# Performance work log

Hardware: AMD Instinct MI355X
Metric: run time of the kernel (lower is better)

The kernel has to match this reference:

```python
import jax, jax.numpy as jnp
import numpy as np

D_MODEL = 1024
N_HEADS = 16
D_K = D_MODEL // N_HEADS
NEG = -1e10


def setup_inputs() -> dict:
    key = jax.random.key(0)
    ks = jax.random.split(key, 12)
    bs, sl = 2, 2048
    q = jax.random.normal(ks[0], (bs, sl, D_MODEL), dtype=jnp.float32)
    k = jax.random.normal(ks[1], (bs, sl, D_MODEL), dtype=jnp.float32)
    v = jax.random.normal(ks[2], (bs, sl, D_MODEL), dtype=jnp.float32)
    mask = jax.random.randint(ks[3], (bs, 1, sl, sl), 0, 2).astype(bool)
    s = 1.0 / np.sqrt(D_MODEL)
    Wq = jax.random.uniform(ks[4], (D_MODEL, D_MODEL), jnp.float32, -s, s)
    bq = jax.random.uniform(ks[5], (D_MODEL,), jnp.float32, -s, s)
    Wk = jax.random.uniform(ks[6], (D_MODEL, D_MODEL), jnp.float32, -s, s)
    bk = jax.random.uniform(ks[7], (D_MODEL,), jnp.float32, -s, s)
    Wv = jax.random.uniform(ks[8], (D_MODEL, D_MODEL), jnp.float32, -s, s)
    bv = jax.random.uniform(ks[9], (D_MODEL,), jnp.float32, -s, s)
    Wo = jax.random.uniform(ks[10], (D_MODEL, D_MODEL), jnp.float32, -s, s)
    bo = jax.random.uniform(ks[11], (D_MODEL,), jnp.float32, -s, s)
    return {"q": q, "k": k, "v": v, "mask": mask,
            "Wq": Wq, "bq": bq, "Wk": Wk, "bk": bk,
            "Wv": Wv, "bv": bv, "Wo": Wo, "bo": bo}


def reference(q, k, v, mask, Wq, bq, Wk, bk, Wv, bv, Wo, bo):
    bs, sl, _ = q.shape
    sl2 = k.shape[1]
    # linear projections (torch Linear: x @ W.T + b), split into heads: [b, h, s, d_k]
    qh = (q @ Wq.T + bq).reshape(bs, sl, N_HEADS, D_K).transpose(0, 2, 1, 3)
    kh = (k @ Wk.T + bk).reshape(bs, sl2, N_HEADS, D_K).transpose(0, 2, 1, 3)
    vh = (v @ Wv.T + bv).reshape(bs, sl2, N_HEADS, D_K).transpose(0, 2, 1, 3)
    scores = jnp.einsum('bhqd,bhkd->bhqk', qh, kh) / jnp.sqrt(jnp.float32(D_K))
    scores = jnp.where(mask, NEG, scores)
    attn = jax.nn.softmax(scores, axis=-1)
    z = jnp.einsum('bhqk,bhkd->bhqd', attn, vh)  # [b, h, sl, d_k]
    z = z.transpose(0, 2, 1, 3).reshape(bs, sl, D_MODEL)
    return z @ Wo.T + bo
```

## Files before the change

### kernel.cpp

```cpp
#include <hip/hip_runtime.h>

typedef __attribute__((ext_vector_type(8))) short short8;
typedef __attribute__((ext_vector_type(4))) float f32x4;

#define MFMA16(a, b, c) __builtin_amdgcn_mfma_f32_16x16x32_bf16((a), (b), (c), 0, 0, 0)

#if __has_builtin(__builtin_amdgcn_exp2f)
#define EXP2(x) __builtin_amdgcn_exp2f(x)
#else
#define EXP2(x) __expf((x) * 0.6931471805599453f)
#endif

__device__ __forceinline__ unsigned short f2bf(float f) {
  unsigned int u = __float_as_uint(f);
  u += 0x7FFFu + ((u >> 16) & 1u);
  return (unsigned short)(u >> 16);
}

__device__ __forceinline__ void gload16(const void* g, void* l) {
  __builtin_amdgcn_global_load_lds((const __attribute__((address_space(1))) void*)g,
                                   (__attribute__((address_space(3))) void*)l, 16, 0, 0);
}

__device__ __forceinline__ short8 fragld64(const unsigned short* base, int row, int kchunk) {
  int cc = kchunk ^ (row & 7);
  return *(const short8*)(base + row * 64 + cc * 8);
}

__device__ __forceinline__ short8 vfragld(const unsigned short* base, int row, int kchunk) {
  int cc = kchunk ^ (row & 7) ^ ((row >> 3) & 7);
  return *(const short8*)(base + row * 64 + cc * 8);
}

__global__ void cvt3(const float* __restrict__ a, const float* __restrict__ b,
                     const float* __restrict__ c, unsigned short* __restrict__ out, int n4) {
  const float* src = (blockIdx.z == 0) ? a : ((blockIdx.z == 1) ? b : c);
  int i = blockIdx.x * blockDim.x + threadIdx.x;
  if (i >= n4) return;
  float4 v = ((const float4*)src)[i];
  ushort4 o;
  o.x = f2bf(v.x); o.y = f2bf(v.y); o.z = f2bf(v.z); o.w = f2bf(v.w);
  ((ushort4*)(out + (size_t)blockIdx.z * (size_t)n4 * 4))[i] = o;
}

__global__ void cvt4(const float* __restrict__ a, const float* __restrict__ b,
                     const float* __restrict__ c, const float* __restrict__ d,
                     unsigned short* __restrict__ out, int n4) {
  const float* src = (blockIdx.z == 0) ? a : ((blockIdx.z == 1) ? b
                   : ((blockIdx.z == 2) ? c : d));
  int i = blockIdx.x * blockDim.x + threadIdx.x;
  if (i >= n4) return;
  float4 v = ((const float4*)src)[i];
  ushort4 o;
  o.x = f2bf(v.x); o.y = f2bf(v.y); o.z = f2bf(v.z); o.w = f2bf(v.w);
  ((ushort4*)(out + (size_t)blockIdx.z * (size_t)n4 * 4))[i] = o;
}

__global__ void maskpack(const int* __restrict__ m, unsigned long long* __restrict__ mw) {
  const int lane = threadIdx.x & 63;
  const size_t wbase = ((size_t)blockIdx.x * (blockDim.x >> 6) + (threadIdx.x >> 6)) * 4ull;
#pragma unroll
  for (int u = 0; u < 4; ++u) {
    size_t word = wbase + u;
    int x = m[word * 64 + lane];
    unsigned long long bb = __ballot(x != 0);
    if (lane == 0) mw[word] = bb;
  }
}

template<bool OUT_BF16>
__global__ __launch_bounds__(256, 3) void gemm_bt(
    const unsigned short* __restrict__ Abase, const unsigned short* __restrict__ Bbase,
    const float* __restrict__ bias0, const float* __restrict__ bias1,
    const float* __restrict__ bias2, void* __restrict__ outv, float scale0)
{
  constexpr int K = 1024, N = 1024;
  const int z = blockIdx.z;
  const unsigned short* A = Abase + (size_t)z * 4194304ull;
  const unsigned short* B = Bbase + (size_t)z * 1048576ull;
  const float* bias = (z == 0) ? bias0 : ((z == 1) ? bias1 : bias2);
  const float scale = (z == 0) ? scale0 : 1.0f;

  __shared__ unsigned short ldsA[128 * 64];
  __shared__ unsigned short ldsB[128 * 64];

  const int tid = threadIdx.x;
  const int lane = tid & 63, wid = tid >> 6;
  const int c16 = lane & 15, g = lane >> 4;
  const int m0 = blockIdx.y * 128, n0 = blockIdx.x * 128;
  const int wr = (wid >> 1) * 64, wc = (wid & 1) * 64;

  f32x4 acc[4][4] = {};

  for (int kt = 0; kt < K; kt += 64) {
    __syncthreads();
#pragma unroll
    for (int i = 0; i < 4; ++i) {
      int row = i * 32 + (tid >> 3);
      int cc = tid & 7;
      int scc = cc ^ (row & 7);
      gload16(A + (size_t)(m0 + row) * K + kt + scc * 8, ldsA + row * 64 + cc * 8);
      gload16(B + (size_t)(n0 + row) * K + kt + scc * 8, ldsB + row * 64 + cc * 8);
    }
    __syncthreads();
#pragma unroll
    for (int kc = 0; kc < 2; ++kc) {
      short8 af[4], bf[4];
#pragma unroll
      for (int mi = 0; mi < 4; ++mi) af[mi] = fragld64(ldsA, wr + mi * 16 + c16, kc * 4 + g);
#pragma unroll
      for (int ni = 0; ni < 4; ++ni) bf[ni] = fragld64(ldsB, wc + ni * 16 + c16, kc * 4 + g);
#pragma unroll
      for (int mi = 0; mi < 4; ++mi)
#pragma unroll
        for (int ni = 0; ni < 4; ++ni)
          acc[mi][ni] = MFMA16(af[mi], bf[ni], acc[mi][ni]);
    }
  }

#pragma unroll
  for (int mi = 0; mi < 4; ++mi)
#pragma unroll
    for (int ni = 0; ni < 4; ++ni) {
      int col = n0 + wc + ni * 16 + c16;
      float bb = bias[col];
#pragma unroll
      for (int r = 0; r < 4; ++r) {
        int row = m0 + wr + mi * 16 + g * 4 + r;
        float v = (acc[mi][ni][r] + bb) * scale;
        if constexpr (OUT_BF16)
          ((unsigned short*)outv)[(size_t)z * 4194304ull + (size_t)row * N + col] = f2bf(v);
        else
          ((float*)outv)[(size_t)row * N + col] = v;
      }
    }
}

__global__ __launch_bounds__(512, 4) void attn(
    const unsigned short* __restrict__ qh, const unsigned short* __restrict__ kh,
    const unsigned short* __restrict__ vh, const unsigned long long* __restrict__ mw,
    unsigned short* __restrict__ zout)
{
  constexpr int SL = 2048, DM = 1024, NT = SL / 64;
  const int q0 = blockIdx.x * 128;
  const int h = blockIdx.y, b = blockIdx.z;
  const int tid = threadIdx.x, lane = tid & 63, w = tid >> 6;
  const int c16 = lane & 15, g = lane >> 4;

  __shared__ unsigned short kbuf[2][4096];
  __shared__ unsigned short vt[2][4096];
  __shared__ unsigned short pbuf[8][1024];

  const int qa = q0 + w * 16;
  const size_t qoff = ((size_t)b * SL + qa + c16) * DM + (size_t)h * 64;
  short8 qf0 = *(const short8*)(qh + qoff + g * 8);
  short8 qf1 = *(const short8*)(qh + qoff + 32 + g * 8);

  f32x4 zacc[4] = {};
  float mrun = -INFINITY, lrun = 0.f;

  const size_t kvbase = (size_t)b * SL * DM + (size_t)h * 64;
  const unsigned long long* mwq = mw + ((size_t)b * SL + qa + c16) * (SL / 64);

  const int krow = tid >> 3, kcc = tid & 7;
  const int vj = tid >> 3, vd0 = (tid & 7) * 8;

  unsigned long long mwc = mwq[0];
  short8 vr;

  gload16(kh + kvbase + (size_t)krow * DM + (kcc ^ (krow & 7)) * 8,
          kbuf[0] + krow * 64 + kcc * 8);
  vr = *(const short8*)(vh + kvbase + (size_t)vj * DM + vd0);
#pragma unroll
  for (int e = 0; e < 8; ++e) {
    int row = vd0 + e;
    int slot = (vj >> 3) ^ (row & 7) ^ ((row >> 3) & 7);
    vt[0][row * 64 + slot * 8 + (vj & 7)] = (unsigned short)vr[e];
  }

  for (int t = 0; t < NT; ++t) {
    const int cur = t & 1, nxt = cur ^ 1;
    __syncthreads();

    const bool more = (t + 1 < NT);
    unsigned long long mwn = 0;
    if (more) {
      const size_t kb = kvbase + (size_t)(t + 1) * 64 * DM;
      gload16(kh + kb + (size_t)krow * DM + (kcc ^ (krow & 7)) * 8,
              kbuf[nxt] + krow * 64 + kcc * 8);
      vr = *(const short8*)(vh + kb + (size_t)vj * DM + vd0);
      mwn = mwq[t + 1];
    }

    f32x4 sacc[4];
#pragma unroll
    for (int nt = 0; nt < 4; ++nt) {
      unsigned int nib = (unsigned int)(mwc >> (nt * 16 + g * 4)) & 0xFu;
#pragma unroll
      for (int r = 0; r < 4; ++r)
        sacc[nt][r] = ((nib >> r) & 1u) ? -1e10f : 0.0f;
    }
#pragma unroll
    for (int kc = 0; kc < 2; ++kc) {
      short8 qfc = kc ? qf1 : qf0;
#pragma unroll
      for (int nt = 0; nt < 4; ++nt) {
        short8 kf = fragld64(kbuf[cur], nt * 16 + c16, kc * 4 + g);
        sacc[nt] = MFMA16(kf, qfc, sacc[nt]);
      }
    }

    float mx;
    {
      float a0 = fmaxf(fmaxf(sacc[0][0], sacc[0][1]), fmaxf(sacc[0][2], sacc[0][3]));
      float a1 = fmaxf(fmaxf(sacc[1][0], sacc[1][1]), fmaxf(sacc[1][2], sacc[1][3]));
      float a2 = fmaxf(fmaxf(sacc[2][0], sacc[2][1]), fmaxf(sacc[2][2], sacc[2][3]));
      float a3 = fmaxf(fmaxf(sacc[3][0], sacc[3][1]), fmaxf(sacc[3][2], sacc[3][3]));
      mx = fmaxf(fmaxf(a0, a1), fmaxf(a2, a3));
    }
    mx = fmaxf(mx, __shfl_xor(mx, 16));
    mx = fmaxf(mx, __shfl_xor(mx, 32));

    const bool defer = __all(mx <= mrun + 8.f) != 0;
    float mnew = defer ? mrun : fmaxf(mrun, mx);
    float rs;
    {
      float ps[4];
#pragma unroll
      for (int nt = 0; nt < 4; ++nt) {
        float p0 = EXP2(sacc[nt][0] - mnew);
        float p1 = EXP2(sacc[nt][1] - mnew);
        float p2 = EXP2(sacc[nt][2] - mnew);
        float p3 = EXP2(sacc[nt][3] - mnew);
        sacc[nt][0] = p0; sacc[nt][1] = p1; sacc[nt][2] = p2; sacc[nt][3] = p3;
        ps[nt] = (p0 + p1) + (p2 + p3);
      }
      rs = (ps[0] + ps[1]) + (ps[2] + ps[3]);
    }
    rs += __shfl_xor(rs, 16);
    rs += __shfl_xor(rs, 32);
    if (defer) {
      lrun += rs;
    } else {
      float alpha = EXP2(mrun - mnew);
      mrun = mnew;
      lrun = lrun * alpha + rs;
#pragma unroll
      for (int r = 0; r < 4; ++r) {
        float ar = __shfl(alpha, g * 4 + r);
        zacc[0][r] *= ar; zacc[1][r] *= ar; zacc[2][r] *= ar; zacc[3][r] *= ar;
      }
    }

    {
      unsigned short* pbw = pbuf[w];
#pragma unroll
      for (int nt = 0; nt < 4; ++nt) {
        int key0 = nt * 16 + g * 4;
        int a16 = c16 * 64 + (((key0 >> 3) ^ (c16 & 7)) * 8) + (key0 & 7);
        unsigned long long pk =
            (unsigned long long)f2bf(sacc[nt][0])
          | ((unsigned long long)f2bf(sacc[nt][1]) << 16)
          | ((unsigned long long)f2bf(sacc[nt][2]) << 32)
          | ((unsigned long long)f2bf(sacc[nt][3]) << 48);
        *(unsigned long long*)(pbw + a16) = pk;
      }
    }

#pragma unroll
    for (int kc = 0; kc < 2; ++kc) {
      short8 pf = fragld64(pbuf[w], c16, kc * 4 + g);
#pragma unroll
      for (int dt = 0; dt < 4; ++dt) {
        short8 vf = vfragld(vt[cur], dt * 16 + c16, kc * 4 + g);
        zacc[dt] = MFMA16(pf, vf, zacc[dt]);
      }
    }

    if (more) {
#pragma unroll
      for (int e = 0; e < 8; ++e) {
        int row = vd0 + e;
        int slot = (vj >> 3) ^ (row & 7) ^ ((row >> 3) & 7);
        vt[nxt][row * 64 + slot * 8 + (vj & 7)] = (unsigned short)vr[e];
      }
      mwc = mwn;
    }
  }

  float invl = 1.f / lrun;
#pragma unroll
  for (int r = 0; r < 4; ++r) {
    float ir = __shfl(invl, g * 4 + r);
    size_t orow = ((size_t)b * SL + qa + g * 4 + r) * DM + (size_t)h * 64;
#pragma unroll
    for (int dt = 0; dt < 4; ++dt)
      zout[orow + dt * 16 + c16] = f2bf(zacc[dt][r] * ir);
  }
}

extern "C" void kernel_launch(void* const* d_in, const int* in_sizes, int n_in,
                              void* d_out, int out_size, void* d_ws, size_t ws_size,
                              hipStream_t stream) {
  const float* q  = (const float*)d_in[0];
  const float* k  = (const float*)d_in[1];
  const float* v  = (const float*)d_in[2];
  const int* mask = (const int*)d_in[3];
  const float* Wq = (const float*)d_in[4];
  const float* bq = (const float*)d_in[5];
  const float* Wk = (const float*)d_in[6];
  const float* bk = (const float*)d_in[7];
  const float* Wv = (const float*)d_in[8];
  const float* bv = (const float*)d_in[9];
  const float* Wo = (const float*)d_in[10];
  const float* bo = (const float*)d_in[11];

  char* ws = (char*)d_ws;
  unsigned short* xbf = (unsigned short*)ws;
  unsigned long long* mwb = (unsigned long long*)ws;
  unsigned short* wbf = (unsigned short*)(ws + 25165824);
  unsigned short* qkv = (unsigned short*)(ws + 33554432);
  unsigned short* zbf = (unsigned short*)(ws + 58720256);

  cvt3<<<dim3(4096, 1, 3), 256, 0, stream>>>(q, k, v, xbf, 1048576);
  cvt4<<<dim3(1024, 1, 4), 256, 0, stream>>>(Wq, Wk, Wv, Wo, wbf, 262144);

  gemm_bt<true><<<dim3(8, 32, 3), 256, 0, stream>>>(xbf, wbf, bq, bk, bv, (void*)qkv,
                                                    0.125f * 1.44269504088896f);
  maskpack<<<8192, 256, 0, stream>>>(mask, mwb);
  attn<<<dim3(16, 16, 2), 512, 0, stream>>>(qkv, qkv + 4194304ull, qkv + 8388608ull, mwb, zbf);
  gemm_bt<false><<<dim3(8, 32, 1), 256, 0, stream>>>(zbf, wbf + 3145728ull, bo, bo, bo, d_out, 1.0f);
}
```

Baseline: 169.6 us.

## Rework attention kernel around 32x32x16 MFMA with 32 queries per wave

The attention kernel switches from 16x16x32 to 32x32x16 bf16 MFMA. Each wave now owns 32 query rows, and blocks shrink from 512 to 128 threads while the grid doubles. The V transpose layout is simplified, P is packed with v_cvt_pk_bf16_f32, and s_setprio is raised around the MFMA sections. This is meant to cut LDS fragment loads and shuffle overhead per FLOP, at the cost of more registers per wave, fewer waves per block, and more K/V staging work per thread.

```diff
diff --git a/kernel.cpp b/kernel.cpp
--- a/kernel.cpp
+++ b/kernel.cpp
@@ -2,8 +2,10 @@
 
 typedef __attribute__((ext_vector_type(8))) short short8;
 typedef __attribute__((ext_vector_type(4))) float f32x4;
+typedef __attribute__((ext_vector_type(16))) float f32x16;
 
 #define MFMA16(a, b, c) __builtin_amdgcn_mfma_f32_16x16x32_bf16((a), (b), (c), 0, 0, 0)
+#define MFMA32(a, b, c) __builtin_amdgcn_mfma_f32_32x32x16_bf16((a), (b), (c), 0, 0, 0)
 
 #if __has_builtin(__builtin_amdgcn_exp2f)
 #define EXP2(x) __builtin_amdgcn_exp2f(x)
@@ -17,6 +19,16 @@
   return (unsigned short)(u >> 16);
 }
 
+__device__ __forceinline__ unsigned int cvtpk(float lo, float hi) {
+  unsigned int r;
+  asm("v_cvt_pk_bf16_f32 %0, %1, %2" : "=v"(r) : "v"(lo), "v"(hi));
+  return r;
+}
+
+__device__ __forceinline__ float fmax3(float a, float b, float c) {
+  return fmaxf(fmaxf(a, b), c);
+}
+
 __device__ __forceinline__ void gload16(const void* g, void* l) {
   __builtin_amdgcn_global_load_lds((const __attribute__((address_space(1))) void*)g,
                                    (__attribute__((address_space(3))) void*)l, 16, 0, 0);
@@ -24,11 +36,6 @@
 
 __device__ __forceinline__ short8 fragld64(const unsigned short* base, int row, int kchunk) {
   int cc = kchunk ^ (row & 7);
-  return *(const short8*)(base + row * 64 + cc * 8);
-}
-
-__device__ __forceinline__ short8 vfragld(const unsigned short* base, int row, int kchunk) {
-  int cc = kchunk ^ (row & 7) ^ ((row >> 3) & 7);
   return *(const short8*)(base + row * 64 + cc * 8);
 }
 
@@ -136,47 +143,58 @@
     }
 }
 
-__global__ __launch_bounds__(512, 4) void attn(
+__global__ __launch_bounds__(128, 2) void attn(
     const unsigned short* __restrict__ qh, const unsigned short* __restrict__ kh,
     const unsigned short* __restrict__ vh, const unsigned long long* __restrict__ mw,
     unsigned short* __restrict__ zout)
 {
   constexpr int SL = 2048, DM = 1024, NT = SL / 64;
-  const int q0 = blockIdx.x * 128;
   const int h = blockIdx.y, b = blockIdx.z;
   const int tid = threadIdx.x, lane = tid & 63, w = tid >> 6;
-  const int c16 = lane & 15, g = lane >> 4;
+  const int ql = lane & 31;
+  const int hd = lane >> 5;
+  const int qa = blockIdx.x * 64 + w * 32;
 
   __shared__ unsigned short kbuf[2][4096];
   __shared__ unsigned short vt[2][4096];
-  __shared__ unsigned short pbuf[8][1024];
-
-  const int qa = q0 + w * 16;
-  const size_t qoff = ((size_t)b * SL + qa + c16) * DM + (size_t)h * 64;
-  short8 qf0 = *(const short8*)(qh + qoff + g * 8);
-  short8 qf1 = *(const short8*)(qh + qoff + 32 + g * 8);
-
-  f32x4 zacc[4] = {};
+  __shared__ unsigned short pbuf[2][2048];
+
+  short8 qf[4];
+  {
+    const size_t qrow = ((size_t)b * SL + qa + ql) * DM + (size_t)h * 64 + hd * 8;
+#pragma unroll
+    for (int kc = 0; kc < 4; ++kc)
+      qf[kc] = *(const short8*)(qh + qrow + kc * 16);
+  }
+
+  f32x16 zacc0 = {}, zacc1 = {};
   float mrun = -INFINITY, lrun = 0.f;
 
   const size_t kvbase = (size_t)b * SL * DM + (size_t)h * 64;
-  const unsigned long long* mwq = mw + ((size_t)b * SL + qa + c16) * (SL / 64);
-
-  const int krow = tid >> 3, kcc = tid & 7;
-  const int vj = tid >> 3, vd0 = (tid & 7) * 8;
+  const unsigned long long* mwq = mw + ((size_t)b * SL + qa + ql) * (SL / 64);
+
+  const int kr0 = tid >> 3, kcc = tid & 7;
+  const int vkey = tid & 63, vdc0 = tid >> 6;
 
   unsigned long long mwc = mwq[0];
-  short8 vr;
-
-  gload16(kh + kvbase + (size_t)krow * DM + (kcc ^ (krow & 7)) * 8,
-          kbuf[0] + krow * 64 + kcc * 8);
-  vr = *(const short8*)(vh + kvbase + (size_t)vj * DM + vd0);
-#pragma unroll
-  for (int e = 0; e < 8; ++e) {
-    int row = vd0 + e;
-    int slot = (vj >> 3) ^ (row & 7) ^ ((row >> 3) & 7);
-    vt[0][row * 64 + slot * 8 + (vj & 7)] = (unsigned short)vr[e];
-  }
+  short8 vr[4];
+
+#pragma unroll
+  for (int i = 0; i < 4; ++i) {
+    int row = kr0 + 16 * i;
+    gload16(kh + kvbase + (size_t)row * DM + (kcc ^ (row & 7)) * 8,
+            kbuf[0] + row * 64 + kcc * 8);
+  }
+#pragma unroll
+  for (int i = 0; i < 4; ++i)
+    vr[i] = *(const short8*)(vh + kvbase + (size_t)vkey * DM + (vdc0 + 2 * i) * 8);
+#pragma unroll
+  for (int i = 0; i < 4; ++i)
+#pragma unroll
+    for (int e = 0; e < 8; ++e) {
+      int row = (vdc0 + 2 * i) * 8 + e;
+      vt[0][row * 64 + (((vkey >> 3) ^ (row & 7)) * 8) + (vkey & 7)] = (unsigned short)vr[i][e];
+    }
 
   for (int t = 0; t < NT; ++t) {
     const int cur = t & 1, nxt = cur ^ 1;
@@ -186,59 +204,85 @@
     unsigned long long mwn = 0;
     if (more) {
       const size_t kb = kvbase + (size_t)(t + 1) * 64 * DM;
-      gload16(kh + kb + (size_t)krow * DM + (kcc ^ (krow & 7)) * 8,
-              kbuf[nxt] + krow * 64 + kcc * 8);
-      vr = *(const short8*)(vh + kb + (size_t)vj * DM + vd0);
+#pragma unroll
+      for (int i = 0; i < 4; ++i) {
+        int row = kr0 + 16 * i;
+        gload16(kh + kb + (size_t)row * DM + (kcc ^ (row & 7)) * 8,
+                kbuf[nxt] + row * 64 + kcc * 8);
+      }
+#pragma unroll
+      for (int i = 0; i < 4; ++i)
+        vr[i] = *(const short8*)(vh + kb + (size_t)vkey * DM + (vdc0 + 2 * i) * 8);
       mwn = mwq[t + 1];
     }
 
-    f32x4 sacc[4];
-#pragma unroll
-    for (int nt = 0; nt < 4; ++nt) {
-      unsigned int nib = (unsigned int)(mwc >> (nt * 16 + g * 4)) & 0xFu;
-#pragma unroll
-      for (int r = 0; r < 4; ++r)
-        sacc[nt][r] = ((nib >> r) & 1u) ? -1e10f : 0.0f;
-    }
-#pragma unroll
-    for (int kc = 0; kc < 2; ++kc) {
-      short8 qfc = kc ? qf1 : qf0;
-#pragma unroll
-      for (int nt = 0; nt < 4; ++nt) {
-        short8 kf = fragld64(kbuf[cur], nt * 16 + c16, kc * 4 + g);
-        sacc[nt] = MFMA16(kf, qfc, sacc[nt]);
+    unsigned int b0 = ((unsigned int)mwc) >> (hd * 4);
+    unsigned int b1 = ((unsigned int)(mwc >> 32)) >> (hd * 4);
+    f32x16 s0, s1;
+#pragma unroll
+    for (int m = 0; m < 4; ++m) {
+      unsigned int n0 = (b0 >> (m * 8)) & 0xFu;
+      unsigned int n1 = (b1 >> (m * 8)) & 0xFu;
+#pragma unroll
+      for (int c = 0; c < 4; ++c) {
+        s0[m * 4 + c] = ((n0 >> c) & 1u) ? -1e10f : 0.0f;
+        s1[m * 4 + c] = ((n1 >> c) & 1u) ? -1e10f : 0.0f;
       }
     }
+
+    __builtin_amdgcn_s_setprio(1);
+#pragma unroll
+    for (int kc = 0; kc < 4; ++kc) {
+      short8 kf0 = fragld64(kbuf[cur], ql, kc * 2 + hd);
+      short8 kf1 = fragld64(kbuf[cur], 32 + ql, kc * 2 + hd);
+      s0 = MFMA32(kf0, qf[kc], s0);
+      s1 = MFMA32(kf1, qf[kc], s1);
+    }
+    __builtin_amdgcn_s_setprio(0);
 
     float mx;
     {
-      float a0 = fmaxf(fmaxf(sacc[0][0], sacc[0][1]), fmaxf(sacc[0][2], sacc[0][3]));
-      float a1 = fmaxf(fmaxf(sacc[1][0], sacc[1][1]), fmaxf(sacc[1][2], sacc[1][3]));
-      float a2 = fmaxf(fmaxf(sacc[2][0], sacc[2][1]), fmaxf(sacc[2][2], sacc[2][3]));
-      float a3 = fmaxf(fmaxf(sacc[3][0], sacc[3][1]), fmaxf(sacc[3][2], sacc[3][3]));
-      mx = fmaxf(fmaxf(a0, a1), fmaxf(a2, a3));
-    }
-    mx = fmaxf(mx, __shfl_xor(mx, 16));
+      float t0 = fmax3(s0[0], s0[1], s0[2]);
+      float t1 = fmax3(s0[3], s0[4], s0[5]);
+      float t2 = fmax3(s0[6], s0[7], s0[8]);
+      float t3 = fmax3(s0[9], s0[10], s0[11]);
+      float t4 = fmax3(s0[12], s0[13], s0[14]);
+      float t5 = fmax3(s0[15], s1[0], s1[1]);
+      float t6 = fmax3(s1[2], s1[3], s1[4]);
+      float t7 = fmax3(s1[5], s1[6], s1[7]);
+      float t8 = fmax3(s1[8], s1[9], s1[10]);
+      float t9 = fmax3(s1[11], s1[12], s1[13]);
+      float ta = fmaxf(s1[14], s1[15]);
+      float u0 = fmax3(t0, t1, t2);
+      float u1 = fmax3(t3, t4, t5);
+      float u2 = fmax3(t6, t7, t8);
+      float u3 = fmaxf(t9, ta);
+      mx = fmaxf(fmax3(u0, u1, u2), u3);
+    }
     mx = fmaxf(mx, __shfl_xor(mx, 32));
 
-    const bool defer = __all(mx <= mrun + 8.f) != 0;
-    float mnew = defer ? mrun : fmaxf(mrun, mx);
+    const bool defer = (__all(mx <= mrun + 8.f) != 0);
+    const float mnew = defer ? mrun : fmaxf(mrun, mx);
+
+#pragma unroll
+    for (int i = 0; i < 16; ++i) {
+      s0[i] = EXP2(s0[i] - mnew);
+      s1[i] = EXP2(s1[i] - mnew);
+    }
     float rs;
     {
-      float ps[4];
-#pragma unroll
-      for (int nt = 0; nt < 4; ++nt) {
-        float p0 = EXP2(sacc[nt][0] - mnew);
-        float p1 = EXP2(sacc[nt][1] - mnew);
-        float p2 = EXP2(sacc[nt][2] - mnew);
-        float p3 = EXP2(sacc[nt][3] - mnew);
-        sacc[nt][0] = p0; sacc[nt][1] = p1; sacc[nt][2] = p2; sacc[nt][3] = p3;
-        ps[nt] = (p0 + p1) + (p2 + p3);
-      }
-      rs = (ps[0] + ps[1]) + (ps[2] + ps[3]);
-    }
-    rs += __shfl_xor(rs, 16);
+      float a0 = (s0[0] + s0[1]) + (s0[2] + s0[3]);
+      float a1 = (s0[4] + s0[5]) + (s0[6] + s0[7]);
+      float a2 = (s0[8] + s0[9]) + (s0[10] + s0[11]);
+      float a3 = (s0[12] + s0[13]) + (s0[14] + s0[15]);
+      float a4 = (s1[0] + s1[1]) + (s1[2] + s1[3]);
+      float a5 = (s1[4] + s1[5]) + (s1[6] + s1[7]);
+      float a6 = (s1[8] + s1[9]) + (s1[10] + s1[11]);
+      float a7 = (s1[12] + s1[13]) + (s1[14] + s1[15]);
+      rs = ((a0 + a1) + (a2 + a3)) + ((a4 + a5) + (a6 + a7));
+    }
     rs += __shfl_xor(rs, 32);
+
     if (defer) {
       lrun += rs;
     } else {
@@ -246,56 +290,64 @@
       mrun = mnew;
       lrun = lrun * alpha + rs;
 #pragma unroll
-      for (int r = 0; r < 4; ++r) {
-        float ar = __shfl(alpha, g * 4 + r);
-        zacc[0][r] *= ar; zacc[1][r] *= ar; zacc[2][r] *= ar; zacc[3][r] *= ar;
+      for (int reg = 0; reg < 16; ++reg) {
+        float ar = __shfl(alpha, (reg & 3) + 8 * (reg >> 2) + 4 * hd);
+        zacc0[reg] *= ar;
+        zacc1[reg] *= ar;
       }
     }
 
     {
       unsigned short* pbw = pbuf[w];
 #pragma unroll
-      for (int nt = 0; nt < 4; ++nt) {
-        int key0 = nt * 16 + g * 4;
-        int a16 = c16 * 64 + (((key0 >> 3) ^ (c16 & 7)) * 8) + (key0 & 7);
-        unsigned long long pk =
-            (unsigned long long)f2bf(sacc[nt][0])
-          | ((unsigned long long)f2bf(sacc[nt][1]) << 16)
-          | ((unsigned long long)f2bf(sacc[nt][2]) << 32)
-          | ((unsigned long long)f2bf(sacc[nt][3]) << 48);
-        *(unsigned long long*)(pbw + a16) = pk;
-      }
-    }
-
-#pragma unroll
-    for (int kc = 0; kc < 2; ++kc) {
-      short8 pf = fragld64(pbuf[w], c16, kc * 4 + g);
-#pragma unroll
-      for (int dt = 0; dt < 4; ++dt) {
-        short8 vf = vfragld(vt[cur], dt * 16 + c16, kc * 4 + g);
-        zacc[dt] = MFMA16(pf, vf, zacc[dt]);
-      }
-    }
+      for (int st = 0; st < 2; ++st)
+#pragma unroll
+        for (int m = 0; m < 4; ++m) {
+          uint2 pk;
+          if (st == 0) {
+            pk.x = cvtpk(s0[m * 4 + 0], s0[m * 4 + 1]);
+            pk.y = cvtpk(s0[m * 4 + 2], s0[m * 4 + 3]);
+          } else {
+            pk.x = cvtpk(s1[m * 4 + 0], s1[m * 4 + 1]);
+            pk.y = cvtpk(s1[m * 4 + 2], s1[m * 4 + 3]);
+          }
+          int chunk = st * 4 + m;
+          int a16 = ql * 64 + ((chunk ^ (ql & 7)) * 8) + hd * 4;
+          *(uint2*)(pbw + a16) = pk;
+        }
+    }
+
+    __builtin_amdgcn_s_setprio(1);
+#pragma unroll
+    for (int kc = 0; kc < 4; ++kc) {
+      short8 pf = fragld64(pbuf[w], ql, kc * 2 + hd);
+      short8 vf0 = fragld64(vt[cur], ql, kc * 2 + hd);
+      short8 vf1 = fragld64(vt[cur], 32 + ql, kc * 2 + hd);
+      zacc0 = MFMA32(pf, vf0, zacc0);
+      zacc1 = MFMA32(pf, vf1, zacc1);
+    }
+    __builtin_amdgcn_s_setprio(0);
 
     if (more) {
 #pragma unroll
-      for (int e = 0; e < 8; ++e) {
-        int row = vd0 + e;
-        int slot = (vj >> 3) ^ (row & 7) ^ ((row >> 3) & 7);
-        vt[nxt][row * 64 + slot * 8 + (vj & 7)] = (unsigned short)vr[e];
-      }
+      for (int i = 0; i < 4; ++i)
+#pragma unroll
+        for (int e = 0; e < 8; ++e) {
+          int row = (vdc0 + 2 * i) * 8 + e;
+          vt[nxt][row * 64 + (((vkey >> 3) ^ (row & 7)) * 8) + (vkey & 7)] = (unsigned short)vr[i][e];
+        }
       mwc = mwn;
     }
   }
 
   float invl = 1.f / lrun;
 #pragma unroll
-  for (int r = 0; r < 4; ++r) {
-    float ir = __shfl(invl, g * 4 + r);
-    size_t orow = ((size_t)b * SL + qa + g * 4 + r) * DM + (size_t)h * 64;
-#pragma unroll
-    for (int dt = 0; dt < 4; ++dt)
-      zout[orow + dt * 16 + c16] = f2bf(zacc[dt][r] * ir);
+  for (int reg = 0; reg < 16; ++reg) {
+    int qrow = (reg & 3) + 8 * (reg >> 2) + 4 * hd;
+    float il = __shfl(invl, qrow);
+    size_t orow = ((size_t)b * SL + qa + qrow) * DM + (size_t)h * 64;
+    zout[orow + ql] = f2bf(zacc0[reg] * il);
+    zout[orow + 32 + ql] = f2bf(zacc1[reg] * il);
   }
 }
 
@@ -328,6 +380,6 @@
   gemm_bt<true><<<dim3(8, 32, 3), 256, 0, stream>>>(xbf, wbf, bq, bk, bv, (void*)qkv,
                                                     0.125f * 1.44269504088896f);
   maskpack<<<8192, 256, 0, stream>>>(mask, mwb);
-  attn<<<dim3(16, 16, 2), 512, 0, stream>>>(qkv, qkv + 4194304ull, qkv + 8388608ull, mwb, zbf);
+  attn<<<dim3(32, 16, 2), 128, 0, stream>>>(qkv, qkv + 4194304ull, qkv + 8388608ull, mwb, zbf);
   gemm_bt<false><<<dim3(8, 32, 1), 256, 0, stream>>>(zbf, wbf + 3145728ull, bo, bo, bo, d_out, 1.0f);
 }
```

Result: slower. 178.4 us (+5.2%).
